# Optimization experiments

Hardware: AMD Instinct MI355X
Metric: run time of the kernel (lower is better)

The kernel has to match this reference:

```python
import jax, jax.numpy as jnp
import numpy as np

B, S, D = 4, 2048, 1024
H = 16
HD = D // H  # head_dim = 64


def setup_inputs() -> dict:
    key = jax.random.key(0)
    ks = jax.random.split(key, 5)
    scale = 1.0 / np.sqrt(D)
    return {
        "x": jax.random.normal(ks[0], (B, S, D), dtype=jnp.float32),
        "Wq": jax.random.normal(ks[1], (D, D), dtype=jnp.float32) * scale,
        "Wk": jax.random.normal(ks[2], (D, D), dtype=jnp.float32) * scale,
        "Wv": jax.random.normal(ks[3], (D, D), dtype=jnp.float32) * scale,
        "Wo": jax.random.normal(ks[4], (D, D), dtype=jnp.float32) * scale,
        "bo": jnp.zeros((D,), dtype=jnp.float32),
    }


def reference(x, Wq, Wk, Wv, Wo, bo):
    b, s, d = x.shape
    # project and split heads: [b, h, s, hd]
    q = (x @ Wq).reshape(b, s, H, HD).transpose(0, 2, 1, 3)
    k = (x @ Wk).reshape(b, s, H, HD).transpose(0, 2, 1, 3)
    v = (x @ Wv).reshape(b, s, H, HD).transpose(0, 2, 1, 3)
    # scores: [b, h, s, s]
    scores = jnp.einsum("bhqd,bhkd->bhqk", q, k)
    # NOTE: original uses tril(diagonal=1) -> allows one future token (off-by-one)
    mask = jnp.tril(jnp.ones((s, s), dtype=bool), k=1)
    scores = jnp.where(mask, scores, -jnp.inf)
    attn = jax.nn.softmax(scores / np.sqrt(HD), axis=-1)
    # dropout p=0.0 (deterministic baseline): identity
    ctx = jnp.einsum("bhqk,bhkd->bhqd", attn, v)
    ctx = ctx.transpose(0, 2, 1, 3).reshape(b, s, d)
    return ctx @ Wo + bo
```

## Files before the change

kernel.cpp:

```cpp
#include <hip/hip_runtime.h>
#include <hip/hip_bf16.h>

#define Bq 4
#define Sq 2048
#define Dq 1024
#define Hq 16
#define HDq 64
#define Mq (Bq*Sq)

typedef unsigned short u16;
typedef __attribute__((ext_vector_type(8))) __bf16 b16x8;
typedef __attribute__((ext_vector_type(4))) float f32x4;
typedef __attribute__((ext_vector_type(4))) unsigned int u32x4;

__device__ inline float bf2f(u16 h){ union{unsigned u; float f;} v; v.u = ((unsigned)h)<<16; return v.f; }
__device__ inline u16 f2bf(float f){ union{float f; unsigned u;} v; v.f=f; unsigned r = v.u + 0x7FFFu + ((v.u>>16)&1u); return (u16)(r>>16); }
__device__ inline u16 truncbf(float f){ union{float f; unsigned u;} v; v.f=f; return (u16)(v.u>>16); }
__device__ inline float ld_elem(const void* p, size_t i, int isf32){
  return isf32 ? ((const float*)p)[i] : bf2f(((const u16*)p)[i]);
}
__device__ inline void ld16(const u16* g, u16* l){
  __builtin_amdgcn_global_load_lds((const __attribute__((address_space(1))) void*)g,
                                   (__attribute__((address_space(3))) void*)l, 16, 0, 0);
}

#if __has_builtin(__builtin_amdgcn_exp2f)
#define EXP2(x) __builtin_amdgcn_exp2f(x)
#else
#define EXP2(x) __expf((x)*0.69314718056f)
#endif
#define SCALE_LOG2E 0.18033688011112042f

__global__ void detect_dtype(const unsigned* __restrict__ x, int* __restrict__ flag){
  __shared__ int cnt;
  if(threadIdx.x==0) cnt=0;
  __syncthreads();
  int local=0;
  for(int i=threadIdx.x;i<2048;i+=256){
    unsigned w = x[i];
    if(((w>>7)&0xFFu)>=0x90u) local++;
    if(((w>>23)&0xFFu)>=0x90u) local++;
  }
  atomicAdd(&cnt, local);
  __syncthreads();
  if(threadIdx.x==0) *flag = (cnt>64) ? 1 : 0;
}

__global__ __launch_bounds__(256) void convert_x(const void* __restrict__ x, u16* __restrict__ xc,
                                                 const int* __restrict__ flag, int n){
  const int f = *flag;
  int i = (blockIdx.x*256 + threadIdx.x)*8;
  if(i>=n) return;
  if(f){
    const float* xf=(const float*)x;
    #pragma unroll
    for(int j=0;j<8;j++) xc[i+j] = f2bf(xf[i+j]);
  } else {
    *(u32x4*)&xc[i] = *(const u32x4*)((const u16*)x + i);
  }
}

__global__ __launch_bounds__(256) void transpose_w(
    const void* __restrict__ W0, const void* __restrict__ W1,
    const void* __restrict__ W2, const void* __restrict__ W3,
    u16* __restrict__ T0, u16* __restrict__ T1,
    u16* __restrict__ T2, u16* __restrict__ T3,
    const int* __restrict__ flag){
  __shared__ u16 tile[64][65];
  const int f = *flag;
  const int z = blockIdx.z;
  const void* src = (z==0)?W0:(z==1)?W1:(z==2)?W2:W3;
  u16*       dst = (z==0)?T0:(z==1)?T1:(z==2)?T2:T3;
  const int t = threadIdx.x;
  const int k0 = blockIdx.x*64, n0 = blockIdx.y*64;
  #pragma unroll
  for(int r=0;r<16;r++){
    int row = r*4 + (t>>6), col = t&63;
    tile[row][col] = f2bf(ld_elem(src, (size_t)(k0+row)*Dq + n0 + col, f));
  }
  __syncthreads();
  #pragma unroll
  for(int r=0;r<16;r++){
    int row = r*4 + (t>>6), col = t&63;
    dst[(size_t)(n0+row)*Dq + k0 + col] = tile[col][row];
  }
}

template<int MODE>
__global__ __launch_bounds__(256) void gemm128(
    const u16* __restrict__ A, const u16* __restrict__ Bt,
    u16* __restrict__ O0, u16* __restrict__ O1, u16* __restrict__ O2,
    void* __restrict__ Og, const void* __restrict__ bias, const int* __restrict__ flag){
  __shared__ u16 Al[128*64];
  __shared__ u16 Bl[128*64];
  const int f = (MODE==1) ? *flag : 0;
  const int t = threadIdx.x;
  const int lane = t & 63, wave = t >> 6;
  const int quad = lane >> 4, l16 = lane & 15;
  const int wr = wave >> 1, wc = wave & 1;
  const int m0 = blockIdx.y*128, n0 = blockIdx.x*128;

  f32x4 acc[4][4] = {};

  for(int k0=0;k0<Dq;k0+=64){
    #pragma unroll
    for(int r=0;r<4;r++){
      int idx = t + (r<<8);
      int row = idx>>3, g = idx&7;
      int csw = (g ^ (row&7))<<3;
      ld16(&A [(size_t)(m0+row)*Dq + k0 + csw], Al + idx*8);
      ld16(&Bt[(size_t)(n0+row)*Dq + k0 + csw], Bl + idx*8);
    }
    __syncthreads();
    #pragma unroll
    for(int ks=0;ks<2;ks++){
      b16x8 af[4], bfr[4];
      #pragma unroll
      for(int i=0;i<4;i++){
        int row = wr*64 + i*16 + l16;
        af[i] = *(const b16x8*)&Al[row*64 + ((((ks<<2)+quad) ^ (row&7))<<3)];
      }
      #pragma unroll
      for(int j=0;j<4;j++){
        int row = wc*64 + j*16 + l16;
        bfr[j] = *(const b16x8*)&Bl[row*64 + ((((ks<<2)+quad) ^ (row&7))<<3)];
      }
      #pragma unroll
      for(int i=0;i<4;i++)
        #pragma unroll
        for(int j=0;j<4;j++)
          acc[i][j] = __builtin_amdgcn_mfma_f32_16x16x32_bf16(af[i], bfr[j], acc[i][j], 0,0,0);
    }
    __syncthreads();
  }

  #pragma unroll
  for(int i=0;i<4;i++){
    #pragma unroll
    for(int j=0;j<4;j++){
      int n = n0 + wc*64 + j*16 + l16;
      #pragma unroll
      for(int r=0;r<4;r++){
        int m = m0 + wr*64 + i*16 + quad*4 + r;
        float c = acc[i][j][r];
        if (MODE==1){
          float c2 = c + ld_elem(bias, n, f);
          if (f) ((float*)Og)[(size_t)m*Dq + n] = c2;
          else   ((u16*)Og)[(size_t)m*Dq + n]   = f2bf(c2);
        } else {
          int z = n >> 10, nn = n & 1023;
          int b = m >> 11, s = m & 2047;
          int h = nn >> 6, hd = nn & 63;
          if (z==0)      O0[(((size_t)(b*Hq + h))*Sq + s)*HDq + hd] = f2bf(c*SCALE_LOG2E);
          else if (z==1) O1[(((size_t)(b*Hq + h))*Sq + s)*HDq + hd] = f2bf(c);
          else           O2[(((size_t)(b*Hq + h))*HDq + hd)*Sq + s] = f2bf(c);
        }
      }
    }
  }
}

__global__ __launch_bounds__(256) void flash_attn(
    const u16* __restrict__ Q, const u16* __restrict__ K,
    const u16* __restrict__ VT, u16* __restrict__ C){
  __shared__ u16 Kt[128*64];
  __shared__ u16 Vt[64*128];
  __shared__ u16 Pl[4][16][72];
  const int t = threadIdx.x;
  const int lane = t&63, wave = t>>6, quad = lane>>4, l16 = lane&15;
  const int p = blockIdx.x, bh = blockIdx.y;
  const int b = bh >> 4, h = bh & 15;
  const int qt[2] = { p, 31 - p };
  int nk[2];
  #pragma unroll
  for(int tt=0;tt<2;tt++){ int v = qt[tt]+2; nk[tt] = (v<32)?v:32; }
  const int nrounds = (nk[1]+1)>>1;
  const u16* Qh = Q  + (size_t)bh*Sq*HDq;
  const u16* Kh = K  + (size_t)bh*Sq*HDq;
  const u16* Vh = VT + (size_t)bh*HDq*Sq;

  b16x8 aq[2][2];
  #pragma unroll
  for(int tt=0;tt<2;tt++){
    const u16* qp = Qh + (size_t)(qt[tt]*64 + wave*16 + l16)*HDq + quad*8;
    aq[tt][0] = *(const b16x8*)qp;
    aq[tt][1] = *(const b16x8*)(qp + 32);
  }
  b16x8 vone;
  #pragma unroll
  for(int i=0;i<8;i++) vone[i] = (__bf16)1.0f;

  const f32x4 fzero = {0.f,0.f,0.f,0.f};
  f32x4 Oa[2][4]; f32x4 lacc[2];
  #pragma unroll
  for(int tt=0;tt<2;tt++){ lacc[tt]=fzero; for(int j=0;j<4;j++) Oa[tt][j]=fzero; }

  for(int kt2=0; kt2<nrounds; kt2++){
    __syncthreads();
    #pragma unroll
    for(int r=0;r<4;r++){
      int idx = t + (r<<8);
      int row = idx>>3, g = idx&7;
      int csw = (g ^ (row&7))<<3;
      ld16(Kh + (size_t)(kt2*128+row)*HDq + csw, Kt + idx*8);
    }
    #pragma unroll
    for(int r=0;r<4;r++){
      int idx = t + (r<<8);
      int row = idx>>4, g = idx&15;
      int csw = (g ^ (row&15))<<3;
      ld16(Vh + (size_t)row*Sq + (size_t)kt2*128 + csw, Vt + idx*8);
    }
    __syncthreads();

    #pragma unroll
    for(int half=0; half<2; half++){
      const int kt = kt2*2 + half;
      #pragma unroll
      for(int tt=0;tt<2;tt++){
        if (kt >= nk[tt]) continue;
        const int qq0 = qt[tt]*64;
        f32x4 sc[4];
        #pragma unroll
        for(int jn=0;jn<4;jn++){
          int krow = half*64 + jn*16 + l16;
          const u16* kp = &Kt[krow*64];
          f32x4 s = fzero;
          b16x8 bk0 = *(const b16x8*)&kp[((quad     ^ (krow&7))<<3)];
          b16x8 bk1 = *(const b16x8*)&kp[(((quad+4) ^ (krow&7))<<3)];
          s = __builtin_amdgcn_mfma_f32_16x16x32_bf16(aq[tt][0], bk0, s, 0,0,0);
          s = __builtin_amdgcn_mfma_f32_16x16x32_bf16(aq[tt][1], bk1, s, 0,0,0);
          sc[jn] = s;
        }
        if (kt < qt[tt]) {
          #pragma unroll
          for(int jn=0;jn<4;jn++)
            #pragma unroll
            for(int r=0;r<4;r++)
              Pl[wave][quad*4+r][jn*16+l16] = truncbf(EXP2(sc[jn][r]));
        } else {
          const int qbase = qq0 + wave*16 + quad*4;
          #pragma unroll
          for(int jn=0;jn<4;jn++){
            int kg = kt*64 + jn*16 + l16;
            #pragma unroll
            for(int r=0;r<4;r++){
              float sv = sc[jn][r];
              if (kg > qbase + r + 1) sv = -__builtin_inff();
              Pl[wave][quad*4+r][jn*16+l16] = truncbf(EXP2(sv));
            }
          }
        }
        #pragma unroll
        for(int ks=0;ks<2;ks++){
          b16x8 ap = *(const b16x8*)&Pl[wave][l16][ks*32 + quad*8];
          int glog = half*8 + ks*4 + quad;
          #pragma unroll
          for(int jd=0;jd<4;jd++){
            int hd = jd*16 + l16;
            b16x8 bv = *(const b16x8*)&Vt[hd*128 + ((glog ^ (hd&15))<<3)];
            Oa[tt][jd] = __builtin_amdgcn_mfma_f32_16x16x32_bf16(ap, bv, Oa[tt][jd], 0,0,0);
          }
          lacc[tt] = __builtin_amdgcn_mfma_f32_16x16x32_bf16(ap, vone, lacc[tt], 0,0,0);
        }
      }
    }
  }
  #pragma unroll
  for(int tt=0;tt<2;tt++){
    const int qq0 = qt[tt]*64;
    #pragma unroll
    for(int r=0;r<4;r++){
      int s = qq0 + wave*16 + quad*4 + r;
      float inv = 1.0f / lacc[tt][r];
      #pragma unroll
      for(int jd=0;jd<4;jd++)
        C[((size_t)(b*Sq + s))*Dq + h*HDq + jd*16 + l16] = f2bf(Oa[tt][jd][r]*inv);
    }
  }
}

extern "C" void kernel_launch(void* const* d_in, const int* in_sizes, int n_in,
                              void* d_out, int out_size, void* d_ws, size_t ws_size,
                              hipStream_t stream){
  const void* x  = d_in[0];
  const void* Wq = d_in[1];
  const void* Wk = d_in[2];
  const void* Wv = d_in[3];
  const void* Wo = d_in[4];
  const void* bo = d_in[5];

  char* ws = (char*)d_ws;
  size_t off = 0;
  auto wsalloc = [&](size_t bytes)->void*{
    void* p = ws + off; off += (bytes + 255) & ~(size_t)255; return p;
  };
  int* flag = (int*)wsalloc(256);
  u16* WqT = (u16*)wsalloc((size_t)Dq*Dq*2);
  u16* WkT = (u16*)wsalloc((size_t)Dq*Dq*2);
  u16* WvT = (u16*)wsalloc((size_t)Dq*Dq*2);
  u16* WoT = (u16*)wsalloc((size_t)Dq*Dq*2);
  u16* xc  = (u16*)wsalloc((size_t)Mq*Dq*2);
  u16* Qb  = (u16*)wsalloc((size_t)Mq*Dq*2);
  u16* Kb  = (u16*)wsalloc((size_t)Mq*Dq*2);
  u16* VTb = (u16*)wsalloc((size_t)Mq*Dq*2);
  u16* Cb  = (u16*)wsalloc((size_t)Mq*Dq*2);

  detect_dtype<<<1, 256, 0, stream>>>((const unsigned*)x, flag);
  convert_x<<<dim3(Mq*Dq/8/256), 256, 0, stream>>>(x, xc, flag, Mq*Dq);
  transpose_w<<<dim3(16,16,4), 256, 0, stream>>>(Wq,Wk,Wv,Wo, WqT,WkT,WvT,WoT, flag);
  gemm128<0><<<dim3(24, Mq/128), 256, 0, stream>>>(xc, WqT, Qb,Kb,VTb, nullptr, nullptr, flag);
  flash_attn<<<dim3(16, Bq*Hq), 256, 0, stream>>>(Qb, Kb, VTb, Cb);
  gemm128<1><<<dim3(Dq/128, Mq/128), 256, 0, stream>>>(Cb, WoT, nullptr,nullptr,nullptr, d_out, bo, flag);
}
```

Measured before the change: 225.2 us.

## Triple-buffer GEMM LDS loads with 256x128 tiles and 512-thread blocks

Replaces the 128x128 GEMM kernel with a 256x128-tile, 512-thread variant. It streams K-tiles through three LDS buffers using direct global-to-LDS loads, so the next tiles are being fetched while the current one is computed. Explicit vmcnt waits and barriers replace the two __syncthreads per K step. MFMA sections are also wrapped in s_setprio to favour the compute waves. The buffers take about 144KB of LDS, so likely only one block fits per CU despite the launch bound of 2, and the output-projection grid shrinks to 256 blocks.

```diff
diff --git a/kernel.cpp b/kernel.cpp
--- a/kernel.cpp
+++ b/kernel.cpp
@@ -87,52 +87,86 @@
 }
 
 template<int MODE>
-__global__ __launch_bounds__(256) void gemm128(
+__global__ __launch_bounds__(512, 2) void gemm256(
     const u16* __restrict__ A, const u16* __restrict__ Bt,
     u16* __restrict__ O0, u16* __restrict__ O1, u16* __restrict__ O2,
     void* __restrict__ Og, const void* __restrict__ bias, const int* __restrict__ flag){
-  __shared__ u16 Al[128*64];
-  __shared__ u16 Bl[128*64];
+  __shared__ u16 Al[3][256*64];
+  __shared__ u16 Bl[3][128*64];
   const int f = (MODE==1) ? *flag : 0;
   const int t = threadIdx.x;
   const int lane = t & 63, wave = t >> 6;
   const int quad = lane >> 4, l16 = lane & 15;
   const int wr = wave >> 1, wc = wave & 1;
-  const int m0 = blockIdx.y*128, n0 = blockIdx.x*128;
+  const int m0 = blockIdx.y*256, n0 = blockIdx.x*128;
+  const int NT = Dq/64;
 
   f32x4 acc[4][4] = {};
 
-  for(int k0=0;k0<Dq;k0+=64){
+  auto stage = [&](int kt, int s){
+    const int k0 = kt<<6;
     #pragma unroll
     for(int r=0;r<4;r++){
-      int idx = t + (r<<8);
+      int idx = t + (r<<9);
       int row = idx>>3, g = idx&7;
       int csw = (g ^ (row&7))<<3;
-      ld16(&A [(size_t)(m0+row)*Dq + k0 + csw], Al + idx*8);
-      ld16(&Bt[(size_t)(n0+row)*Dq + k0 + csw], Bl + idx*8);
-    }
-    __syncthreads();
+      ld16(&A[(size_t)(m0+row)*Dq + k0 + csw], &Al[s][idx*8]);
+    }
+    #pragma unroll
+    for(int r=0;r<2;r++){
+      int idx = t + (r<<9);
+      int row = idx>>3, g = idx&7;
+      int csw = (g ^ (row&7))<<3;
+      ld16(&Bt[(size_t)(n0+row)*Dq + k0 + csw], &Bl[s][idx*8]);
+    }
+  };
+
+  auto compute = [&](int s){
+    const u16* As = &Al[s][0];
+    const u16* Bs = &Bl[s][0];
     #pragma unroll
     for(int ks=0;ks<2;ks++){
       b16x8 af[4], bfr[4];
       #pragma unroll
       for(int i=0;i<4;i++){
         int row = wr*64 + i*16 + l16;
-        af[i] = *(const b16x8*)&Al[row*64 + ((((ks<<2)+quad) ^ (row&7))<<3)];
+        af[i] = *(const b16x8*)&As[row*64 + ((((ks<<2)+quad) ^ (row&7))<<3)];
       }
       #pragma unroll
       for(int j=0;j<4;j++){
         int row = wc*64 + j*16 + l16;
-        bfr[j] = *(const b16x8*)&Bl[row*64 + ((((ks<<2)+quad) ^ (row&7))<<3)];
+        bfr[j] = *(const b16x8*)&Bs[row*64 + ((((ks<<2)+quad) ^ (row&7))<<3)];
       }
+      __builtin_amdgcn_s_setprio(1);
       #pragma unroll
       for(int i=0;i<4;i++)
         #pragma unroll
         for(int j=0;j<4;j++)
           acc[i][j] = __builtin_amdgcn_mfma_f32_16x16x32_bf16(af[i], bfr[j], acc[i][j], 0,0,0);
-    }
-    __syncthreads();
-  }
+      __builtin_amdgcn_s_setprio(0);
+    }
+  };
+
+  stage(0,0);
+  stage(1,1);
+  asm volatile("s_waitcnt vmcnt(6)" ::: "memory");
+  __builtin_amdgcn_s_barrier();
+  __builtin_amdgcn_sched_barrier(0);
+
+  int s0=0, s1=1, s2=2;
+  for(int tt=0; tt<NT-2; ++tt){
+    stage(tt+2, s2);
+    compute(s0);
+    asm volatile("s_waitcnt vmcnt(6)" ::: "memory");
+    __builtin_amdgcn_s_barrier();
+    __builtin_amdgcn_sched_barrier(0);
+    int x=s0; s0=s1; s1=s2; s2=x;
+  }
+  compute(s0);
+  asm volatile("s_waitcnt vmcnt(0)" ::: "memory");
+  __builtin_amdgcn_s_barrier();
+  __builtin_amdgcn_sched_barrier(0);
+  compute(s1);
 
   #pragma unroll
   for(int i=0;i<4;i++){
@@ -309,7 +343,7 @@
   detect_dtype<<<1, 256, 0, stream>>>((const unsigned*)x, flag);
   convert_x<<<dim3(Mq*Dq/8/256), 256, 0, stream>>>(x, xc, flag, Mq*Dq);
   transpose_w<<<dim3(16,16,4), 256, 0, stream>>>(Wq,Wk,Wv,Wo, WqT,WkT,WvT,WoT, flag);
-  gemm128<0><<<dim3(24, Mq/128), 256, 0, stream>>>(xc, WqT, Qb,Kb,VTb, nullptr, nullptr, flag);
+  gemm256<0><<<dim3(24, Mq/256), 512, 0, stream>>>(xc, WqT, Qb,Kb,VTb, nullptr, nullptr, flag);
   flash_attn<<<dim3(16, Bq*Hq), 256, 0, stream>>>(Qb, Kb, VTb, Cb);
-  gemm128<1><<<dim3(Dq/128, Mq/128), 256, 0, stream>>>(Cb, WoT, nullptr,nullptr,nullptr, d_out, bo, flag);
-}
+  gemm256<1><<<dim3(Dq/128, Mq/256), 512, 0, stream>>>(Cb, WoT, nullptr,nullptr,nullptr, d_out, bo, flag);
+}
```

Result: slower. 238.6 us (+5.9%).

## Triple-buffer GEMM with explicit waitcnt pipelining, larger QKV tiles and XCD-aware block mapping

Applied to the files above, without the earlier changes.

The GEMM kernels now use a three-stage LDS ring of 32-wide K tiles loaded with async global-to-LDS copies. Explicit vmcnt/lgkmcnt waits, barriers and setprio let loads for tile k+2 overlap MFMA work on tile k. The QKV projection uses 256-row tiles so each B fragment is reused across more MFMAs. Block indices for both GEMMs and flash attention are remapped so consecutive blocks on the same XCD (L&7) share A/B panels or heads, aiming for better L2 locality. The cost is tricky hand-written wait counts, larger register use under a 2-blocks launch bound, and fragile assumptions about grid sizes.

```diff
diff --git a/kernel.cpp b/kernel.cpp
--- a/kernel.cpp
+++ b/kernel.cpp
@@ -87,70 +87,148 @@
 }
 
 template<int MODE>
-__global__ __launch_bounds__(256) void gemm128(
+__global__ __launch_bounds__(256, 2) void gemm2p(
     const u16* __restrict__ A, const u16* __restrict__ Bt,
     u16* __restrict__ O0, u16* __restrict__ O1, u16* __restrict__ O2,
     void* __restrict__ Og, const void* __restrict__ bias, const int* __restrict__ flag){
-  __shared__ u16 Al[128*64];
-  __shared__ u16 Bl[128*64];
+  constexpr int BM = (MODE==0)?256:128;
+  constexpr int MF = (MODE==0)?8:4;
+  constexpr int NT = Dq/32;
+  __shared__ u16 Asl[3][BM*32];
+  __shared__ u16 Bsl[3][128*32];
   const int f = (MODE==1) ? *flag : 0;
   const int t = threadIdx.x;
   const int lane = t & 63, wave = t >> 6;
   const int quad = lane >> 4, l16 = lane & 15;
   const int wr = wave >> 1, wc = wave & 1;
-  const int m0 = blockIdx.y*128, n0 = blockIdx.x*128;
-
-  f32x4 acc[4][4] = {};
-
-  for(int k0=0;k0<Dq;k0+=64){
-    #pragma unroll
-    for(int r=0;r<4;r++){
+  int L = blockIdx.x + blockIdx.y*gridDim.x;
+  int k8 = L & 7, ii = L >> 3;
+  int m0, n0;
+  if (MODE==0){
+    int nsb = ii >> 5, rem = ii & 31;
+    int mg = rem >> 3, ng = rem & 7;
+    m0 = (k8*4 + mg)*256; n0 = (nsb*8 + ng)*128;
+  } else {
+    int mg = ii >> 3, ng = ii & 7;
+    m0 = (k8*8 + mg)*128; n0 = ng*128;
+  }
+
+  f32x4 acc[MF][4] = {};
+
+  auto stageA = [&](int T, int s){
+    #pragma unroll
+    for(int r=0;r<BM/64;r++){
       int idx = t + (r<<8);
-      int row = idx>>3, g = idx&7;
-      int csw = (g ^ (row&7))<<3;
-      ld16(&A [(size_t)(m0+row)*Dq + k0 + csw], Al + idx*8);
-      ld16(&Bt[(size_t)(n0+row)*Dq + k0 + csw], Bl + idx*8);
-    }
-    __syncthreads();
-    #pragma unroll
-    for(int ks=0;ks<2;ks++){
-      b16x8 af[4], bfr[4];
-      #pragma unroll
-      for(int i=0;i<4;i++){
-        int row = wr*64 + i*16 + l16;
-        af[i] = *(const b16x8*)&Al[row*64 + ((((ks<<2)+quad) ^ (row&7))<<3)];
-      }
-      #pragma unroll
-      for(int j=0;j<4;j++){
-        int row = wc*64 + j*16 + l16;
-        bfr[j] = *(const b16x8*)&Bl[row*64 + ((((ks<<2)+quad) ^ (row&7))<<3)];
-      }
+      int row = idx>>2, g = idx&3;
+      int gl = g ^ ((row>>1)&3);
+      ld16(&A[(size_t)(m0+row)*Dq + (T<<5) + gl*8], &Asl[s][idx*8]);
+    }
+  };
+  auto stageB = [&](int T, int s){
+    #pragma unroll
+    for(int r=0;r<2;r++){
+      int idx = t + (r<<8);
+      int row = idx>>2, g = idx&3;
+      int gl = g ^ ((row>>1)&3);
+      ld16(&Bt[(size_t)(n0+row)*Dq + (T<<5) + gl*8], &Bsl[s][idx*8]);
+    }
+  };
+  auto ldA = [&](int s, int i)->b16x8{
+    int row = wr*(MF*16) + i*16 + l16;
+    return *(const b16x8*)&Asl[s][row*32 + ((quad ^ ((row>>1)&3))<<3)];
+  };
+  auto ldB = [&](int s, int j)->b16x8{
+    int row = wc*64 + j*16 + l16;
+    return *(const b16x8*)&Bsl[s][row*32 + ((quad ^ ((row>>1)&3))<<3)];
+  };
+  #define MFMA_BF16 __builtin_amdgcn_mfma_f32_16x16x32_bf16
+
+  stageA(0,0); stageB(0,0); stageA(1,1); stageB(1,1);
+  if (MODE==0) asm volatile("s_waitcnt vmcnt(6)" ::: "memory");
+  else         asm volatile("s_waitcnt vmcnt(4)" ::: "memory");
+  __builtin_amdgcn_s_barrier();
+  __builtin_amdgcn_sched_barrier(0);
+
+  int s0=0, s1=1, s2=2;
+  for(int tt=0; tt<NT; ++tt){
+    if (MODE==0){
+      if(tt+2<NT) stageA(tt+2, s2);
+      b16x8 af[4], bf[4];
+      #pragma unroll
+      for(int i=0;i<4;i++) af[i]=ldA(s0,i);
+      #pragma unroll
+      for(int j=0;j<4;j++) bf[j]=ldB(s0,j);
+      __builtin_amdgcn_s_barrier();
+      asm volatile("s_waitcnt lgkmcnt(0)" ::: "memory");
+      __builtin_amdgcn_sched_barrier(0);
+      __builtin_amdgcn_s_setprio(1);
       #pragma unroll
       for(int i=0;i<4;i++)
         #pragma unroll
         for(int j=0;j<4;j++)
-          acc[i][j] = __builtin_amdgcn_mfma_f32_16x16x32_bf16(af[i], bfr[j], acc[i][j], 0,0,0);
-    }
-    __syncthreads();
-  }
-
-  #pragma unroll
-  for(int i=0;i<4;i++){
+          acc[i][j]=MFMA_BF16(af[i],bf[j],acc[i][j],0,0,0);
+      __builtin_amdgcn_s_setprio(0);
+      __builtin_amdgcn_s_barrier();
+      __builtin_amdgcn_sched_barrier(0);
+      if(tt+2<NT) stageB(tt+2, s2);
+      #pragma unroll
+      for(int i=0;i<4;i++) af[i]=ldA(s0,4+i);
+      __builtin_amdgcn_s_barrier();
+      asm volatile("s_waitcnt lgkmcnt(0)" ::: "memory");
+      __builtin_amdgcn_sched_barrier(0);
+      __builtin_amdgcn_s_setprio(1);
+      #pragma unroll
+      for(int i=0;i<4;i++)
+        #pragma unroll
+        for(int j=0;j<4;j++)
+          acc[4+i][j]=MFMA_BF16(af[i],bf[j],acc[4+i][j],0,0,0);
+      __builtin_amdgcn_s_setprio(0);
+      if(tt<NT-2) asm volatile("s_waitcnt vmcnt(6)" ::: "memory");
+      else        asm volatile("s_waitcnt vmcnt(0)" ::: "memory");
+      __builtin_amdgcn_s_barrier();
+      __builtin_amdgcn_sched_barrier(0);
+    } else {
+      if(tt+2<NT){ stageA(tt+2, s2); stageB(tt+2, s2); }
+      b16x8 af[4], bf[4];
+      #pragma unroll
+      for(int i=0;i<4;i++) af[i]=ldA(s0,i);
+      #pragma unroll
+      for(int j=0;j<4;j++) bf[j]=ldB(s0,j);
+      __builtin_amdgcn_s_barrier();
+      asm volatile("s_waitcnt lgkmcnt(0)" ::: "memory");
+      __builtin_amdgcn_sched_barrier(0);
+      __builtin_amdgcn_s_setprio(1);
+      #pragma unroll
+      for(int i=0;i<4;i++)
+        #pragma unroll
+        for(int j=0;j<4;j++)
+          acc[i][j]=MFMA_BF16(af[i],bf[j],acc[i][j],0,0,0);
+      __builtin_amdgcn_s_setprio(0);
+      if(tt<NT-2) asm volatile("s_waitcnt vmcnt(4)" ::: "memory");
+      else        asm volatile("s_waitcnt vmcnt(0)" ::: "memory");
+      __builtin_amdgcn_s_barrier();
+      __builtin_amdgcn_sched_barrier(0);
+    }
+    int x=s0; s0=s1; s1=s2; s2=x;
+  }
+
+  #pragma unroll
+  for(int i=0;i<MF;i++){
     #pragma unroll
     for(int j=0;j<4;j++){
       int n = n0 + wc*64 + j*16 + l16;
       #pragma unroll
       for(int r=0;r<4;r++){
-        int m = m0 + wr*64 + i*16 + quad*4 + r;
+        int m = m0 + wr*(MF*16) + i*16 + quad*4 + r;
         float c = acc[i][j][r];
         if (MODE==1){
           float c2 = c + ld_elem(bias, n, f);
           if (f) ((float*)Og)[(size_t)m*Dq + n] = c2;
           else   ((u16*)Og)[(size_t)m*Dq + n]   = f2bf(c2);
         } else {
-          int z = n >> 10, nn = n & 1023;
+          int z = n >> 10, nn2 = n & 1023;
           int b = m >> 11, s = m & 2047;
-          int h = nn >> 6, hd = nn & 63;
+          int h = nn2 >> 6, hd = nn2 & 63;
           if (z==0)      O0[(((size_t)(b*Hq + h))*Sq + s)*HDq + hd] = f2bf(c*SCALE_LOG2E);
           else if (z==1) O1[(((size_t)(b*Hq + h))*Sq + s)*HDq + hd] = f2bf(c);
           else           O2[(((size_t)(b*Hq + h))*HDq + hd)*Sq + s] = f2bf(c);
@@ -158,6 +236,7 @@
       }
     }
   }
+  #undef MFMA_BF16
 }
 
 __global__ __launch_bounds__(256) void flash_attn(
@@ -168,7 +247,10 @@
   __shared__ u16 Pl[4][16][72];
   const int t = threadIdx.x;
   const int lane = t&63, wave = t>>6, quad = lane>>4, l16 = lane&15;
-  const int p = blockIdx.x, bh = blockIdx.y;
+  int L  = blockIdx.x + blockIdx.y*gridDim.x;
+  int k8 = L & 7, ii = L >> 3;
+  const int bh = k8*8 + (ii>>4);
+  const int p  = ii & 15;
   const int b = bh >> 4, h = bh & 15;
   const int qt[2] = { p, 31 - p };
   int nk[2];
@@ -309,7 +391,7 @@
   detect_dtype<<<1, 256, 0, stream>>>((const unsigned*)x, flag);
   convert_x<<<dim3(Mq*Dq/8/256), 256, 0, stream>>>(x, xc, flag, Mq*Dq);
   transpose_w<<<dim3(16,16,4), 256, 0, stream>>>(Wq,Wk,Wv,Wo, WqT,WkT,WvT,WoT, flag);
-  gemm128<0><<<dim3(24, Mq/128), 256, 0, stream>>>(xc, WqT, Qb,Kb,VTb, nullptr, nullptr, flag);
+  gemm2p<0><<<dim3(24, 32), 256, 0, stream>>>(xc, WqT, Qb,Kb,VTb, nullptr, nullptr, flag);
   flash_attn<<<dim3(16, Bq*Hq), 256, 0, stream>>>(Qb, Kb, VTb, Cb);
-  gemm128<1><<<dim3(Dq/128, Mq/128), 256, 0, stream>>>(Cb, WoT, nullptr,nullptr,nullptr, d_out, bo, flag);
-}
+  gemm2p<1><<<dim3(8, 64), 256, 0, stream>>>(Cb, WoT, nullptr,nullptr,nullptr, d_out, bo, flag);
+}
```

Result: faster. 208.3 us (-7.5%).
